# Performance work log

Hardware: AMD Instinct MI355X
Metric: run time of the kernel (lower is better)

## Reference

```python
import jax, jax.numpy as jnp
import numpy as np

N = 50000
E = 250000
NUM_ETYPES = 4
H = 2  # num_heads
EPS = 1e-12


def _gat_conv(x, W, al, ar, b, src, dst):
    # x: (N, in_dim); W: (in_dim, H*D); al/ar/b: (H, D); src/dst: (E,)
    D = al.shape[-1]
    feat = (x @ W).reshape(-1, H, D)            # (N, H, D)
    el = jnp.sum(feat * al, axis=-1)            # (N, H)
    er = jnp.sum(feat * ar, axis=-1)            # (N, H)
    e = jax.nn.leaky_relu(el[src] + er[dst], 0.2)   # (E, H)
    emax = jax.ops.segment_max(e, dst, num_segments=N)
    ex = jnp.exp(e - emax[dst])
    denom = jax.ops.segment_sum(ex, dst, num_segments=N)
    alpha = ex / denom[dst]                     # (E, H) segment softmax over in-edges
    msg = feat[src] * alpha[:, :, None]         # (E, H, D)
    out = jax.ops.segment_sum(msg, dst, num_segments=N)  # (N, H, D)
    return out + b


def _hetero_layer(x, W, al, ar, b, edges):
    # vmap GATConv over the edge-type axis, then HeteroGraphConv aggregate='mean'
    outs = jax.vmap(lambda w, a, r, bb, e: _gat_conv(x, w, a, r, bb, e[0], e[1]))(
        W, al, ar, b, edges)                    # (T, N, H, D)
    return jnp.mean(outs, axis=0)               # (N, H, D)


def _post(v):
    # relu -> F.normalize(dim=1, i.e. across heads) -> dropout(eval: identity) -> mean over heads
    v = jax.nn.relu(v)
    norm = jnp.sqrt(jnp.sum(v * v, axis=1, keepdims=True))
    v = v / jnp.maximum(norm, EPS)
    return jnp.mean(v, axis=1)                  # (N, D)


def setup_inputs() -> dict:
    key = jax.random.key(0)
    ks = jax.random.split(key, 16)
    s = 0.05
    inp = {
        'x': jax.random.normal(ks[0], (N, 23), jnp.float32),
        'edges': jax.random.randint(ks[1], (NUM_ETYPES, 2, E), 0, N, jnp.int32),
        'W0': jax.random.normal(ks[2], (NUM_ETYPES, 23, H * 64), jnp.float32) * s,
        'al0': jax.random.normal(ks[3], (NUM_ETYPES, H, 64), jnp.float32) * s,
        'ar0': jax.random.normal(ks[4], (NUM_ETYPES, H, 64), jnp.float32) * s,
        'b0': jnp.zeros((NUM_ETYPES, H, 64), jnp.float32),
        'W1': jax.random.normal(ks[5], (NUM_ETYPES, 64, H * 64), jnp.float32) * s,
        'al1': jax.random.normal(ks[6], (NUM_ETYPES, H, 64), jnp.float32) * s,
        'ar1': jax.random.normal(ks[7], (NUM_ETYPES, H, 64), jnp.float32) * s,
        'b1': jnp.zeros((NUM_ETYPES, H, 64), jnp.float32),
        'W2': jax.random.normal(ks[8], (NUM_ETYPES, 64, H * 64), jnp.float32) * s,
        'al2': jax.random.normal(ks[9], (NUM_ETYPES, H, 64), jnp.float32) * s,
        'ar2': jax.random.normal(ks[10], (NUM_ETYPES, H, 64), jnp.float32) * s,
        'b2': jnp.zeros((NUM_ETYPES, H, 64), jnp.float32),
    }
    return inp


def reference(x, edges, W0, al0, ar0, b0, W1, al1, ar1, b1, W2, al2, ar2, b2):
    h = x  # feature_by_level, feat_level=0
    h = _post(_hetero_layer(h, W0, al0, ar0, b0, edges))
    h = _post(_hetero_layer(h, W1, al1, ar1, b1, edges))
    h = jnp.mean(_hetero_layer(h, W2, al2, ar2, b2, edges), axis=1)  # (N, out_dim)
    out = jnp.mean(h, axis=0, keepdims=True)    # dgl.mean_nodes, single graph -> (1, out_dim)
    return out
```

## Files before the change

### kernel.cpp

```cpp
#include <hip/hip_runtime.h>

#define NN 50000
#define NE 250000
#define NSCAN_BLKS ((NN + 255)/256)
#define EDGE_BLKS ((4*NE + 255)/256)
#define NBUCK 4
#define BSZ ((NN + NBUCK - 1)/NBUCK)

typedef __attribute__((ext_vector_type(8))) short bf16x8;
typedef __attribute__((ext_vector_type(4))) float f32x4;

__device__ inline ushort f2bf(float f) {
  uint u = __float_as_uint(f);
  return (ushort)((u + 0x7fffu + ((u >> 16) & 1u)) >> 16);
}
__device__ inline float bf2f(ushort b) { return __uint_as_float(((uint)b) << 16); }

__global__ __launch_bounds__(256) void zero_ints(int* __restrict__ p, int n) {
  int i = blockIdx.x*256 + threadIdx.x;
  if (i < n) p[i] = 0;
}
__global__ __launch_bounds__(256) void zero_floats(float* __restrict__ p, int n) {
  int i = blockIdx.x*256 + threadIdx.x;
  if (i < n) p[i] = 0.f;
}

__global__ __launch_bounds__(256) void count_kernel(const int* __restrict__ edges, int* __restrict__ counts) {
  int idx = blockIdx.x*256 + threadIdx.x;
  if (idx >= 4*NE) return;
  int t = idx / NE, e = idx - t*NE;
  int dst = edges[(size_t)t*2*NE + NE + e];
  atomicAdd(&counts[t*NN + dst], 1);
}

__global__ __launch_bounds__(256) void sumdeg_kernel(const int* __restrict__ counts, int* __restrict__ totdeg) {
  int v = blockIdx.x*256 + threadIdx.x;
  if (v < NN) totdeg[v] = counts[v] + counts[NN+v] + counts[2*NN+v] + counts[3*NN+v];
}

__global__ __launch_bounds__(256) void scan1_kernel(const int* __restrict__ in, int* __restrict__ out, int* __restrict__ bsum, int n) {
  __shared__ int sd[256];
  int i = blockIdx.x*256 + threadIdx.x;
  int v = (i < n) ? in[i] : 0;
  sd[threadIdx.x] = v;
  __syncthreads();
  for (int off = 1; off < 256; off <<= 1) {
    int add = (threadIdx.x >= off) ? sd[threadIdx.x - off] : 0;
    __syncthreads();
    sd[threadIdx.x] += add;
    __syncthreads();
  }
  if (i < n) out[i] = sd[threadIdx.x] - v;
  if (threadIdx.x == 255) bsum[blockIdx.x] = sd[255];
}

__global__ __launch_bounds__(1024) void scan2_kernel(int* __restrict__ bsum, int nb) {
  __shared__ int sd[1024];
  int i = threadIdx.x;
  int v = (i < nb) ? bsum[i] : 0;
  sd[i] = v;
  __syncthreads();
  for (int off = 1; off < 1024; off <<= 1) {
    int add = (i >= off) ? sd[i - off] : 0;
    __syncthreads();
    sd[i] += add;
    __syncthreads();
  }
  if (i < nb) bsum[i] = sd[i] - v;
}

__global__ __launch_bounds__(256) void scan3b_kernel(int* __restrict__ rp, const int* __restrict__ bsum, int n, int total) {
  int i = blockIdx.x*256 + threadIdx.x;
  if (i < n) rp[i] += bsum[blockIdx.x];
  if (i == 0) rp[n] = total;
}

__global__ __launch_bounds__(256) void make_cursor_kernel(const int* __restrict__ rp2, const int* __restrict__ counts,
                                                          int* __restrict__ cursor, int* __restrict__ sub_ptr) {
  int v = blockIdx.x*256 + threadIdx.x;
  if (v >= NN) return;
  int b = rp2[v];
  int s1 = b  + counts[v];
  int s2 = s1 + counts[NN+v];
  int s3 = s2 + counts[2*NN+v];
  cursor[v] = b; cursor[NN+v] = s1; cursor[2*NN+v] = s2; cursor[3*NN+v] = s3;
  sub_ptr[NN+v] = s1; sub_ptr[2*NN+v] = s2; sub_ptr[3*NN+v] = s3;
}

__global__ __launch_bounds__(256) void scatter_bucketed(const int* __restrict__ edges, int* __restrict__ cursor,
                                                        int* __restrict__ col2) {
  const int b = blockIdx.x / EDGE_BLKS;
  const int idx = (blockIdx.x - b*EDGE_BLKS)*256 + threadIdx.x;
  if (idx >= 4*NE) return;
  const int t = idx / NE, e = idx - t*NE;
  const int dst = edges[(size_t)t*2*NE + NE + e];
  if (dst < b*BSZ || dst >= (b+1)*BSZ) return;
  const int src = edges[(size_t)t*2*NE + e];
  const int pos = atomicAdd(&cursor[t*NN + dst], 1);
  col2[pos] = src;
}

__global__ __launch_bounds__(256) void convert_x_kernel(const float* __restrict__ x, ushort* __restrict__ xpad) {
  int i = blockIdx.x*256 + threadIdx.x;
  if (i >= NN*64) return;
  int k = i & 63, n = i >> 6;
  xpad[i] = (k < 23) ? f2bf(x[n*23 + k]) : (ushort)0;
}

__global__ __launch_bounds__(256) void convert_wb3_kernel(const float* __restrict__ W0, const float* __restrict__ W1,
                                                          const float* __restrict__ W2, ushort* __restrict__ WB3) {
  int i = blockIdx.x*256 + threadIdx.x;
  if (i >= 3*4*128*64) return;
  int l = i / (4*128*64); int r = i - l*(4*128*64);
  int k = r & 63, c = (r >> 6) & 127, t = r >> 13;
  const float* W = (l == 0) ? W0 : (l == 1) ? W1 : W2;
  const int Kin = (l == 0) ? 23 : 64;
  float w = (k < Kin) ? W[((size_t)t*Kin + k)*128 + c] : 0.f;
  WB3[i] = f2bf(w);
}

__global__ __launch_bounds__(256) void walwar3_kernel(const float* __restrict__ W0, const float* __restrict__ W1,
                                                      const float* __restrict__ W2, const float* __restrict__ al0,
                                                      const float* __restrict__ al1, const float* __restrict__ al2,
                                                      const float* __restrict__ ar0, const float* __restrict__ ar1,
                                                      const float* __restrict__ ar2, ushort* __restrict__ wwb3) {
  int i = blockIdx.x*256 + threadIdx.x;
  if (i >= 3*16*64) return;
  int l = i / (16*64); int r = i - l*(16*64);
  int c = r >> 6, k = r & 63;
  int lr = c >> 3, t = (c >> 1) & 3, h = c & 1;
  const float* W  = (l == 0) ? W0 : (l == 1) ? W1 : W2;
  const float* al = (l == 0) ? al0 : (l == 1) ? al1 : al2;
  const float* ar = (l == 0) ? ar0 : (l == 1) ? ar1 : ar2;
  const int Kin = (l == 0) ? 23 : 64;
  float v = 0.f;
  if (k < Kin) {
    const float* A = (lr ? ar : al) + t*128 + h*64;
    const float* wr = W + ((size_t)t*Kin + k)*128 + h*64;
    for (int d = 0; d < 64; ++d) v += wr[d]*A[d];
  }
  wwb3[i] = f2bf(v);
}

__global__ __launch_bounds__(256)
void elk_kernel(const ushort* __restrict__ hbf, const ushort* __restrict__ wwb,
                float* __restrict__ elp, float* __restrict__ erp)
{
  __shared__ ushort BS[16*64];
  __shared__ float sC[16*66];
  const int tid = threadIdx.x;
  if (tid < 128) ((bf16x8*)BS)[tid] = ((const bf16x8*)wwb)[tid];
  __syncthreads();

  const int wv = tid >> 6, lane = tid & 63;
  const int mrow = lane & 15, kq = lane >> 4;
  const int anode = blockIdx.x*64 + wv*16 + mrow;

  const bf16x8 a0 = *(const bf16x8*)(hbf + (size_t)anode*64 + kq*8);
  const bf16x8 a1 = *(const bf16x8*)(hbf + (size_t)anode*64 + 32 + kq*8);
  const bf16x8 b0 = *(const bf16x8*)(BS + mrow*64 + kq*8);
  const bf16x8 b1 = *(const bf16x8*)(BS + mrow*64 + 32 + kq*8);

  f32x4 acc = (f32x4){0.f,0.f,0.f,0.f};
  acc = __builtin_amdgcn_mfma_f32_16x16x32_bf16(a0, b0, acc, 0, 0, 0);
  acc = __builtin_amdgcn_mfma_f32_16x16x32_bf16(a1, b1, acc, 0, 0, 0);

  #pragma unroll
  for (int r = 0; r < 4; ++r) sC[mrow*66 + wv*16 + kq*4 + r] = acc[r];
  __syncthreads();

  const int t = tid >> 6, n = tid & 63;
  const int node = blockIdx.x*64 + n;
  if (node < NN) {
    float2 e2 = make_float2(sC[(t*2+0)*66 + n], sC[(t*2+1)*66 + n]);
    float2 r2 = make_float2(sC[(8+t*2+0)*66 + n], sC[(8+t*2+1)*66 + n]);
    ((float2*)elp)[(size_t)t*NN + node] = e2;
    ((float2*)erp)[(size_t)t*NN + node] = r2;
  }
}

__global__ __launch_bounds__(256)
void gather_kernel(const ushort* __restrict__ hbf, const float* __restrict__ elp,
                   const float* __restrict__ erp, const int* __restrict__ col2,
                   const int* __restrict__ row_ptr2, const int* __restrict__ sub_ptr,
                   ushort* __restrict__ agg)
{
  const int v = __builtin_amdgcn_readfirstlane(blockIdx.x*4 + (threadIdx.x >> 6));
  const int lane = threadIdx.x & 63;
  const int h2 = lane >> 5;
  const int j  = lane & 31;
  const uint* hb32 = (const uint*)hbf;
  uint* agg32 = (uint*)agg;

  const int b0 = row_ptr2[v];
  const int b4 = row_ptr2[v+1];
  const int s1 = sub_ptr[NN+v], s2 = sub_ptr[2*NN+v], s3 = sub_ptr[3*NN+v];
  const int bounds[5] = {b0, s1, s2, s3, b4};

  #pragma unroll
  for (int t = 0; t < 4; ++t) {
    const int lo = bounds[t], hi = bounds[t+1];
    float ox = 0.f, oy = 0.f;
    if (lo < hi) {
      const float2 er2 = ((const float2*)erp)[(size_t)t*NN + v];
      float sum0 = 0.f, sum1 = 0.f, tx0 = 0.f, ty0 = 0.f, tx1 = 0.f, ty1 = 0.f;
      #pragma unroll 2
      for (int q = lo + h2; q < hi; q += 2) {
        const int src = col2[q];
        const float2 e2 = ((const float2*)elp)[(size_t)t*NN + src];
        float u0 = e2.x + er2.x, u1 = e2.y + er2.y;
        u0 = (u0 > 0.f) ? u0 : 0.2f*u0;
        u1 = (u1 > 0.f) ? u1 : 0.2f*u1;
        const float p0 = __expf(fminf(u0, 80.f));
        const float p1 = __expf(fminf(u1, 80.f));
        sum0 += p0; sum1 += p1;
        const uint w = hb32[(uint)src*32u + (uint)j];
        const float xv0 = __uint_as_float(w << 16);
        const float xv1 = __uint_as_float(w & 0xffff0000u);
        tx0 += p0*xv0; ty0 += p0*xv1;
        tx1 += p1*xv0; ty1 += p1*xv1;
      }
      sum0 += __shfl_xor(sum0, 32); sum1 += __shfl_xor(sum1, 32);
      tx0 += __shfl_xor(tx0, 32);   ty0 += __shfl_xor(ty0, 32);
      tx1 += __shfl_xor(tx1, 32);   ty1 += __shfl_xor(ty1, 32);
      const float i0 = __builtin_amdgcn_rcpf(sum0);
      const float i1 = __builtin_amdgcn_rcpf(sum1);
      ox = h2 ? tx1*i1 : tx0*i0;
      oy = h2 ? ty1*i1 : ty0*i0;
    }
    const uint pk = (uint)f2bf(ox) | ((uint)f2bf(oy) << 16);
    __builtin_nontemporal_store(pk, &agg32[(size_t)(t*NN + v)*64 + h2*32 + j]);
  }
}

__global__ __launch_bounds__(256)
void transform_kernel(const ushort* __restrict__ agg, const ushort* __restrict__ WB,
                      const float* __restrict__ ball, ushort* __restrict__ hout, int post)
{
  __shared__ ushort WT[2*128*64];
  __shared__ float sb[128];
  const int tid = threadIdx.x;
  if (tid < 128) sb[tid] = 0.25f*(ball[tid] + ball[128+tid] + ball[256+tid] + ball[384+tid]);

  const int wv = tid >> 6, lane = tid & 63;
  const int mrow = lane & 15, kq = lane >> 4;
  const int node0 = blockIdx.x*128;
  const int anode0 = node0 + wv*32 + mrow;

  f32x4 acc[2][8];
  #pragma unroll
  for (int m = 0; m < 2; ++m)
    #pragma unroll
    for (int nb = 0; nb < 8; ++nb) acc[m][nb] = (f32x4){0.f,0.f,0.f,0.f};

  for (int tb = 0; tb < 4; tb += 2) {
    __syncthreads();
    for (int i = tid; i < 2048; i += 256) {
      int row = i >> 3, jj = i & 7;
      bf16x8 val = ((const bf16x8*)WB)[tb*1024 + i];
      *(bf16x8*)((char*)WT + row*128 + ((jj ^ (row & 7))*16)) = val;
    }
    __syncthreads();
    #pragma unroll
    for (int t2 = 0; t2 < 2; ++t2) {
      const int t = tb + t2;
      bf16x8 a[2][4];
      #pragma unroll
      for (int m = 0; m < 2; ++m) {
        const ushort* ar_ = agg + ((size_t)t*NN + anode0 + m*16)*128;
        a[m][0] = __builtin_nontemporal_load((const bf16x8*)(ar_ + kq*8));
        a[m][1] = __builtin_nontemporal_load((const bf16x8*)(ar_ + 32 + kq*8));
        a[m][2] = __builtin_nontemporal_load((const bf16x8*)(ar_ + 64 + kq*8));
        a[m][3] = __builtin_nontemporal_load((const bf16x8*)(ar_ + 96 + kq*8));
      }
      #pragma unroll
      for (int nb = 0; nb < 8; ++nb) {
        const int row = t2*128 + nb*16 + mrow;
        const bf16x8 b0 = *(const bf16x8*)((const char*)WT + row*128 + ((kq       ^ (row&7))*16));
        const bf16x8 b1 = *(const bf16x8*)((const char*)WT + row*128 + (((4 + kq) ^ (row&7))*16));
        const int hs = (nb >> 2)*2;
        #pragma unroll
        for (int m = 0; m < 2; ++m) {
          acc[m][nb] = __builtin_amdgcn_mfma_f32_16x16x32_bf16(a[m][hs],   b0, acc[m][nb], 0, 0, 0);
          acc[m][nb] = __builtin_amdgcn_mfma_f32_16x16x32_bf16(a[m][hs+1], b1, acc[m][nb], 0, 0, 0);
        }
      }
    }
  }

  #pragma unroll
  for (int m = 0; m < 2; ++m) {
    const int noder = node0 + wv*32 + m*16 + kq*4;
    #pragma unroll
    for (int nb = 0; nb < 4; ++nb) {
      const int d = nb*16 + mrow;
      const float bm0 = sb[d], bm1 = sb[64 + d];
      #pragma unroll
      for (int r = 0; r < 4; ++r) {
        if (noder + r < NN) {
          float h0 = 0.25f*acc[m][nb][r]   + bm0;
          float h1 = 0.25f*acc[m][nb+4][r] + bm1;
          float o;
          if (post) {
            h0 = fmaxf(h0, 0.f); h1 = fmaxf(h1, 0.f);
            o = 0.5f*(h0 + h1) / fmaxf(sqrtf(h0*h0 + h1*h1), 1e-12f);
          } else {
            o = 0.5f*(h0 + h1);
          }
          hout[(size_t)(noder + r)*64 + d] = f2bf(o);
        }
      }
    }
  }
}

__global__ __launch_bounds__(256) void reduce_nodes(const ushort* __restrict__ hn, float* __restrict__ accum) {
  __shared__ float sd[256];
  int d = threadIdx.x & 63, rg = threadIdx.x >> 6;
  float s = 0.f;
  for (int r = blockIdx.x*4 + rg; r < NN; r += gridDim.x*4) s += bf2f(hn[(size_t)r*64 + d]);
  sd[threadIdx.x] = s;
  __syncthreads();
  if (threadIdx.x < 64) {
    s = sd[threadIdx.x] + sd[threadIdx.x+64] + sd[threadIdx.x+128] + sd[threadIdx.x+192];
    atomicAdd(&accum[threadIdx.x], s);
  }
}
__global__ __launch_bounds__(64) void final_out_kernel(const float* __restrict__ accum, float* __restrict__ out) {
  int d = threadIdx.x;
  if (d < 64) out[d] = accum[d] * (1.0f/NN);
}

extern "C" void kernel_launch(void* const* d_in, const int* in_sizes, int n_in,
                              void* d_out, int out_size, void* d_ws, size_t ws_size,
                              hipStream_t stream) {
  const float* x     = (const float*)d_in[0];
  const int*   edges = (const int*)d_in[1];
  const float* W[3]  = {(const float*)d_in[2], (const float*)d_in[6], (const float*)d_in[10]};
  const float* al[3] = {(const float*)d_in[3], (const float*)d_in[7], (const float*)d_in[11]};
  const float* ar[3] = {(const float*)d_in[4], (const float*)d_in[8], (const float*)d_in[12]};
  const float* b[3]  = {(const float*)d_in[5], (const float*)d_in[9], (const float*)d_in[13]};

  char* ws = (char*)d_ws;
  auto up = [](size_t x_) { return (x_ + 255) & ~(size_t)255; };

  const size_t szAgg  = ((size_t)4*NN + 128)*128*sizeof(ushort);
  const size_t szElp  = (size_t)4*NN*2*sizeof(float);
  const size_t szHB   = (size_t)(NN+64)*64*sizeof(ushort);
  const size_t szWB3  = (size_t)3*4*128*64*sizeof(ushort);
  const size_t szWWB3 = (size_t)3*16*64*sizeof(ushort);
  const size_t szCol  = (size_t)4*NE*sizeof(int);
  const size_t szI4   = (size_t)4*NN*sizeof(int);
  const size_t szI1   = (size_t)(NN+1)*sizeof(int);

  size_t o = 0;
  ushort* agg    = (ushort*)(ws + o); o += up(szAgg);
  float*  elp    = (float*)(ws + o);  o += up(szElp);
  float*  erp    = (float*)(ws + o);  o += up(szElp);
  ushort* xpad   = (ushort*)(ws + o); o += up(szHB);
  ushort* hbuf   = (ushort*)(ws + o); o += up(szHB);
  ushort* WB3    = (ushort*)(ws + o); o += up(szWB3);
  ushort* wwb3   = (ushort*)(ws + o); o += up(szWWB3);
  float*  accum  = (float*)(ws + o);  o += up(256);
  int*    col2   = (int*)(ws + o);    o += up(szCol);
  int* row_ptr2  = (int*)(ws + o);    o += up(szI1);
  int* totdeg    = (int*)(ws + o);    o += up(szI1);
  int* cursor    = (int*)(ws + o);    o += up(szI4);
  int* counts    = (int*)(ws + o);    o += up(szI4);
  int* sub_ptr   = (int*)(ws + o);    o += up(szI4);
  int* bsum      = (int*)(ws + o);    o += up(4096);

  convert_wb3_kernel<<<(3*4*128*64 + 255)/256, 256, 0, stream>>>(W[0], W[1], W[2], WB3);
  walwar3_kernel<<<(3*16*64 + 255)/256, 256, 0, stream>>>(W[0], W[1], W[2], al[0], al[1], al[2],
                                                          ar[0], ar[1], ar[2], wwb3);
  convert_x_kernel<<<(NN*64 + 255)/256, 256, 0, stream>>>(x, xpad);

  zero_ints<<<(4*NN + 255)/256, 256, 0, stream>>>(counts, 4*NN);
  count_kernel<<<EDGE_BLKS, 256, 0, stream>>>(edges, counts);
  sumdeg_kernel<<<NSCAN_BLKS, 256, 0, stream>>>(counts, totdeg);
  scan1_kernel<<<NSCAN_BLKS, 256, 0, stream>>>(totdeg, row_ptr2, bsum, NN);
  scan2_kernel<<<1, 1024, 0, stream>>>(bsum, NSCAN_BLKS);
  scan3b_kernel<<<NSCAN_BLKS, 256, 0, stream>>>(row_ptr2, bsum, NN, 4*NE);
  make_cursor_kernel<<<NSCAN_BLKS, 256, 0, stream>>>(row_ptr2, counts, cursor, sub_ptr);
  scatter_bucketed<<<NBUCK*EDGE_BLKS, 256, 0, stream>>>(edges, cursor, col2);

  const int gemmGX = (NN + 63)/64;
  const int tfGX   = (NN + 127)/128;

  for (int l = 0; l < 3; ++l) {
    const ushort* hin = (l == 0) ? xpad : hbuf;
    const ushort* WB  = WB3 + (size_t)l*4*128*64;
    const ushort* wwb = wwb3 + (size_t)l*16*64;
    elk_kernel<<<gemmGX, 256, 0, stream>>>(hin, wwb, elp, erp);
    gather_kernel<<<NN/4, 256, 0, stream>>>(hin, elp, erp, col2, row_ptr2, sub_ptr, agg);
    transform_kernel<<<tfGX, 256, 0, stream>>>(agg, WB, b[l], hbuf, (l < 2) ? 1 : 0);
  }

  zero_floats<<<1, 64, 0, stream>>>(accum, 64);
  reduce_nodes<<<256, 256, 0, stream>>>(hbuf, accum);
  final_out_kernel<<<1, 64, 0, stream>>>(accum, (float*)d_out);
}
```

Before: 392.5 us.

## Fuse next-layer attention logits and final node reduction into transform kernel

Result: faster. 376.0 us (-4.2%).

```diff
diff --git a/kernel.cpp b/kernel.cpp
--- a/kernel.cpp
+++ b/kernel.cpp
@@ -76,7 +76,7 @@
 }
 
 __global__ __launch_bounds__(256) void make_cursor_kernel(const int* __restrict__ rp2, const int* __restrict__ counts,
-                                                          int* __restrict__ cursor, int* __restrict__ sub_ptr) {
+                                                          int* __restrict__ cursor, int4* __restrict__ bnd4) {
   int v = blockIdx.x*256 + threadIdx.x;
   if (v >= NN) return;
   int b = rp2[v];
@@ -84,7 +84,8 @@
   int s2 = s1 + counts[NN+v];
   int s3 = s2 + counts[2*NN+v];
   cursor[v] = b; cursor[NN+v] = s1; cursor[2*NN+v] = s2; cursor[3*NN+v] = s3;
-  sub_ptr[NN+v] = s1; sub_ptr[2*NN+v] = s2; sub_ptr[3*NN+v] = s3;
+  bnd4[v] = make_int4(b, s1, s2, s3);
+  if (v == 0) bnd4[NN] = make_int4(4*NE, 4*NE, 4*NE, 4*NE);
 }
 
 __global__ __launch_bounds__(256) void scatter_bucketed(const int* __restrict__ edges, int* __restrict__ cursor,
@@ -182,8 +183,7 @@
 __global__ __launch_bounds__(256)
 void gather_kernel(const ushort* __restrict__ hbf, const float* __restrict__ elp,
                    const float* __restrict__ erp, const int* __restrict__ col2,
-                   const int* __restrict__ row_ptr2, const int* __restrict__ sub_ptr,
-                   ushort* __restrict__ agg)
+                   const int4* __restrict__ bnd4, ushort* __restrict__ agg)
 {
   const int v = __builtin_amdgcn_readfirstlane(blockIdx.x*4 + (threadIdx.x >> 6));
   const int lane = threadIdx.x & 63;
@@ -192,10 +192,9 @@
   const uint* hb32 = (const uint*)hbf;
   uint* agg32 = (uint*)agg;
 
-  const int b0 = row_ptr2[v];
-  const int b4 = row_ptr2[v+1];
-  const int s1 = sub_ptr[NN+v], s2 = sub_ptr[2*NN+v], s3 = sub_ptr[3*NN+v];
-  const int bounds[5] = {b0, s1, s2, s3, b4};
+  const int4 bb = bnd4[v];
+  const int b4 = ((const int*)bnd4)[(v+1)*4];
+  const int bounds[5] = {bb.x, bb.y, bb.z, bb.w, b4};
 
   #pragma unroll
   for (int t = 0; t < 4; ++t) {
@@ -235,10 +234,14 @@
 
 __global__ __launch_bounds__(256)
 void transform_kernel(const ushort* __restrict__ agg, const ushort* __restrict__ WB,
-                      const float* __restrict__ ball, ushort* __restrict__ hout, int post)
+                      const float* __restrict__ ball, ushort* __restrict__ hout, int post,
+                      const ushort* __restrict__ wwbN, float* __restrict__ elp,
+                      float* __restrict__ erp, float* __restrict__ accum, int doReduce)
 {
   __shared__ ushort WT[2*128*64];
+  __shared__ ushort oS[128][72];
   __shared__ float sb[128];
+  __shared__ float sred[256];
   const int tid = threadIdx.x;
   if (tid < 128) sb[tid] = 0.25f*(ball[tid] + ball[128+tid] + ball[256+tid] + ball[384+tid]);
 
@@ -290,42 +293,70 @@
 
   #pragma unroll
   for (int m = 0; m < 2; ++m) {
-    const int noder = node0 + wv*32 + m*16 + kq*4;
+    const int nl0 = wv*32 + m*16 + kq*4;
     #pragma unroll
     for (int nb = 0; nb < 4; ++nb) {
       const int d = nb*16 + mrow;
       const float bm0 = sb[d], bm1 = sb[64 + d];
       #pragma unroll
       for (int r = 0; r < 4; ++r) {
-        if (noder + r < NN) {
-          float h0 = 0.25f*acc[m][nb][r]   + bm0;
-          float h1 = 0.25f*acc[m][nb+4][r] + bm1;
-          float o;
-          if (post) {
-            h0 = fmaxf(h0, 0.f); h1 = fmaxf(h1, 0.f);
-            o = 0.5f*(h0 + h1) / fmaxf(sqrtf(h0*h0 + h1*h1), 1e-12f);
-          } else {
-            o = 0.5f*(h0 + h1);
-          }
-          hout[(size_t)(noder + r)*64 + d] = f2bf(o);
+        float h0 = 0.25f*acc[m][nb][r]   + bm0;
+        float h1 = 0.25f*acc[m][nb+4][r] + bm1;
+        float o;
+        if (post) {
+          h0 = fmaxf(h0, 0.f); h1 = fmaxf(h1, 0.f);
+          o = 0.5f*(h0 + h1) / fmaxf(sqrtf(h0*h0 + h1*h1), 1e-12f);
+        } else {
+          o = 0.5f*(h0 + h1);
         }
+        oS[nl0 + r][d] = f2bf(o);
       }
     }
   }
-}
-
-__global__ __launch_bounds__(256) void reduce_nodes(const ushort* __restrict__ hn, float* __restrict__ accum) {
-  __shared__ float sd[256];
-  int d = threadIdx.x & 63, rg = threadIdx.x >> 6;
-  float s = 0.f;
-  for (int r = blockIdx.x*4 + rg; r < NN; r += gridDim.x*4) s += bf2f(hn[(size_t)r*64 + d]);
-  sd[threadIdx.x] = s;
   __syncthreads();
-  if (threadIdx.x < 64) {
-    s = sd[threadIdx.x] + sd[threadIdx.x+64] + sd[threadIdx.x+128] + sd[threadIdx.x+192];
-    atomicAdd(&accum[threadIdx.x], s);
-  }
-}
+
+  if (hout) {
+    for (int i = tid; i < 128*16; i += 256) {
+      const int nl = i >> 4, seg = i & 15;
+      const int v = node0 + nl;
+      if (v < NN) *(ushort4*)&hout[(size_t)v*64 + seg*4] = *(ushort4*)&oS[nl][seg*4];
+    }
+  }
+
+  if (wwbN) {
+    #pragma unroll
+    for (int m2 = 0; m2 < 2; ++m2) {
+      const int ng = wv*2 + m2;
+      const int arow = ng*16 + mrow;
+      const bf16x8 a0 = *(const bf16x8*)&oS[arow][kq*8];
+      const bf16x8 a1 = *(const bf16x8*)&oS[arow][32 + kq*8];
+      const bf16x8 b0 = *(const bf16x8*)(wwbN + mrow*64 + kq*8);
+      const bf16x8 b1 = *(const bf16x8*)(wwbN + mrow*64 + 32 + kq*8);
+      f32x4 c = (f32x4){0.f,0.f,0.f,0.f};
+      c = __builtin_amdgcn_mfma_f32_16x16x32_bf16(a0, b0, c, 0, 0, 0);
+      c = __builtin_amdgcn_mfma_f32_16x16x32_bf16(a1, b1, c, 0, 0, 0);
+      const int lr = mrow >> 3, t = (mrow >> 1) & 3, h = mrow & 1;
+      float* dst = lr ? erp : elp;
+      #pragma unroll
+      for (int r = 0; r < 4; ++r) {
+        const int v = node0 + ng*16 + kq*4 + r;
+        if (v < NN) dst[((size_t)t*NN + v)*2 + h] = c[r];
+      }
+    }
+  }
+
+  if (doReduce) {
+    const int d = tid & 63, g = tid >> 6;
+    float s = 0.f;
+    for (int nl = g; nl < 128; nl += 4)
+      if (node0 + nl < NN) s += bf2f(oS[nl][d]);
+    sred[tid] = s;
+    __syncthreads();
+    if (tid < 64)
+      atomicAdd(&accum[tid], sred[tid] + sred[tid+64] + sred[tid+128] + sred[tid+192]);
+  }
+}
+
 __global__ __launch_bounds__(64) void final_out_kernel(const float* __restrict__ accum, float* __restrict__ out) {
   int d = threadIdx.x;
   if (d < 64) out[d] = accum[d] * (1.0f/NN);
@@ -350,6 +381,7 @@
   const size_t szWB3  = (size_t)3*4*128*64*sizeof(ushort);
   const size_t szWWB3 = (size_t)3*16*64*sizeof(ushort);
   const size_t szCol  = (size_t)4*NE*sizeof(int);
+  const size_t szBnd  = (size_t)(NN+1)*sizeof(int4);
   const size_t szI4   = (size_t)4*NN*sizeof(int);
   const size_t szI1   = (size_t)(NN+1)*sizeof(int);
 
@@ -363,11 +395,11 @@
   ushort* wwb3   = (ushort*)(ws + o); o += up(szWWB3);
   float*  accum  = (float*)(ws + o);  o += up(256);
   int*    col2   = (int*)(ws + o);    o += up(szCol);
+  int4*   bnd4   = (int4*)(ws + o);   o += up(szBnd);
   int* row_ptr2  = (int*)(ws + o);    o += up(szI1);
   int* totdeg    = (int*)(ws + o);    o += up(szI1);
   int* cursor    = (int*)(ws + o);    o += up(szI4);
   int* counts    = (int*)(ws + o);    o += up(szI4);
-  int* sub_ptr   = (int*)(ws + o);    o += up(szI4);
   int* bsum      = (int*)(ws + o);    o += up(4096);
 
   convert_wb3_kernel<<<(3*4*128*64 + 255)/256, 256, 0, stream>>>(W[0], W[1], W[2], WB3);
@@ -381,22 +413,25 @@
   scan1_kernel<<<NSCAN_BLKS, 256, 0, stream>>>(totdeg, row_ptr2, bsum, NN);
   scan2_kernel<<<1, 1024, 0, stream>>>(bsum, NSCAN_BLKS);
   scan3b_kernel<<<NSCAN_BLKS, 256, 0, stream>>>(row_ptr2, bsum, NN, 4*NE);
-  make_cursor_kernel<<<NSCAN_BLKS, 256, 0, stream>>>(row_ptr2, counts, cursor, sub_ptr);
+  make_cursor_kernel<<<NSCAN_BLKS, 256, 0, stream>>>(row_ptr2, counts, cursor, bnd4);
   scatter_bucketed<<<NBUCK*EDGE_BLKS, 256, 0, stream>>>(edges, cursor, col2);
+  zero_floats<<<1, 64, 0, stream>>>(accum, 64);
 
   const int gemmGX = (NN + 63)/64;
   const int tfGX   = (NN + 127)/128;
+
+  elk_kernel<<<gemmGX, 256, 0, stream>>>(xpad, wwb3, elp, erp);
 
   for (int l = 0; l < 3; ++l) {
     const ushort* hin = (l == 0) ? xpad : hbuf;
     const ushort* WB  = WB3 + (size_t)l*4*128*64;
-    const ushort* wwb = wwb3 + (size_t)l*16*64;
-    elk_kernel<<<gemmGX, 256, 0, stream>>>(hin, wwb, elp, erp);
-    gather_kernel<<<NN/4, 256, 0, stream>>>(hin, elp, erp, col2, row_ptr2, sub_ptr, agg);
-    transform_kernel<<<tfGX, 256, 0, stream>>>(agg, WB, b[l], hbuf, (l < 2) ? 1 : 0);
-  }
-
-  zero_floats<<<1, 64, 0, stream>>>(accum, 64);
-  reduce_nodes<<<256, 256, 0, stream>>>(hbuf, accum);
+    const ushort* wwbNext = (l < 2) ? (wwb3 + (size_t)(l+1)*16*64) : nullptr;
+    gather_kernel<<<NN/4, 256, 0, stream>>>(hin, elp, erp, col2, bnd4, agg);
+    transform_kernel<<<tfGX, 256, 0, stream>>>(agg, WB, b[l],
+                                               (l < 2) ? hbuf : nullptr, (l < 2) ? 1 : 0,
+                                               wwbNext, elp, erp,
+                                               accum, (l == 2) ? 1 : 0);
+  }
+
   final_out_kernel<<<1, 64, 0, stream>>>(accum, (float*)d_out);
 }
```
